# Kernel tuning notes

Measured on AMD Instinct MI355X. Metric: run time of the kernel, lower is better.

The kernel has to match this reference:

```python
import jax, jax.numpy as jnp
import numpy as np
from jax import lax

H, W = 128, 128
K_JUNC = 300
STEPS = 32
THRESH = 0.008
BIAS_SPAN = 1
SCALE = 5.0
SENTINEL = K_JUNC * K_JUNC


def decode_hafm(angs, dist, bias):
    # angs [B,3,H,W], dist [B,1,H,W], bias [B,1,H,W] -> lines [B,3,H,W,4]
    bias_range = jnp.arange(-BIAS_SPAN, BIAS_SPAN + 1, dtype=jnp.float32).reshape(1, -1, 1, 1)
    d = jnp.clip(dist + bias * bias_range, 0.0, 1.0)  # [B,3,H,W]
    angle0 = (angs[:, 0:1] - 0.5) * jnp.pi * 2
    angle1 = angs[:, 1:2] * jnp.pi / 2
    angle2 = -angs[:, 2:3] * jnp.pi / 2
    c0, s0 = jnp.cos(angle0), jnp.sin(angle0)
    t1, t2 = jnp.tan(angle1), jnp.tan(angle2)
    x1 = (c0 - s0 * t1) * d * SCALE
    y1 = (s0 + c0 * t1) * d * SCALE
    x2 = (c0 - s0 * t2) * d * SCALE
    y2 = (s0 + c0 * t2) * d * SCALE
    y0, x0 = jnp.meshgrid(jnp.arange(H, dtype=jnp.float32), jnp.arange(W, dtype=jnp.float32), indexing='ij')
    x0 = x0[None, None]
    y0 = y0[None, None]
    x1 = jnp.clip(x1 + x0, 0, W - 1)
    y1 = jnp.clip(y1 + y0, 0, H - 1)
    x2 = jnp.clip(x2 + x0, 0, W - 1)
    y2 = jnp.clip(y2 + y0, 0, H - 1)
    return jnp.stack((x1, y1, x2, y2), axis=-1)


def propose_junctions(jloc, joff):
    # jloc [H,W], joff [2,H,W]; 3x3 NMS + top-K, thresholded junctions
    pooled = lax.reduce_window(jloc, -jnp.inf, lax.max, (3, 3), (1, 1), 'SAME')
    nms = jnp.where(jloc == pooled, jloc, 0.0)
    scores, idx = lax.top_k(nms.reshape(-1), K_JUNC)
    y = (idx // W).astype(jnp.float32)
    x = (idx % W).astype(jnp.float32)
    xs = x + joff[0].reshape(-1)[idx]
    ys = y + joff[1].reshape(-1)[idx]
    coords = jnp.stack([xs, ys], axis=-1)  # [K,2]
    valid = scores > THRESH
    coords = jnp.where(valid[:, None], coords, 1e6)
    return coords, scores


def bilinear_sample(fmap, px, py):
    # fmap [C,H,W]; px,py [N,S] -> [C,N,S]
    C = fmap.shape[0]
    px = jnp.clip(px, 0.0, W - 1)
    py = jnp.clip(py, 0.0, H - 1)
    x0 = jnp.floor(px)
    y0 = jnp.floor(py)
    x0i = x0.astype(jnp.int32)
    y0i = y0.astype(jnp.int32)
    x1i = jnp.minimum(x0i + 1, W - 1)
    y1i = jnp.minimum(y0i + 1, H - 1)
    wx = px - x0
    wy = py - y0
    flat = fmap.reshape(C, H * W)

    def g(yi, xi):
        return flat[:, (yi * W + xi).reshape(-1)].reshape(C, *px.shape)

    return (g(y0i, x0i) * (1 - wx) * (1 - wy)
            + g(y0i, x1i) * wx * (1 - wy)
            + g(y1i, x0i) * (1 - wx) * wy
            + g(y1i, x1i) * wx * wy)


def setup_inputs() -> dict:
    key = jax.random.key(0)
    ks = jax.random.split(key, 10)
    return {
        'features': jax.random.normal(ks[0], (1, 256, H, W), jnp.float32),
        'heatmaps': jax.random.normal(ks[1], (1, 9, H, W), jnp.float32),
        'fc1_w': jax.random.normal(ks[2], (128, 256), jnp.float32) * 0.05,
        'fc1_b': jax.random.normal(ks[3], (128,), jnp.float32) * 0.05,
        'w1': jax.random.normal(ks[4], (1024, 1024), jnp.float32) * 0.03,
        'b1': jnp.zeros((1024,), jnp.float32),
        'w2': jax.random.normal(ks[5], (1024, 1024), jnp.float32) * 0.03,
        'b2': jnp.zeros((1024,), jnp.float32),
        'w3': jax.random.normal(ks[6], (1, 1024), jnp.float32) * 0.03,
        'b3': jnp.zeros((1,), jnp.float32),
    }


def reference(features, heatmaps, fc1_w, fc1_b, w1, b1, w2, b2, w3, b3):
    angs = jax.nn.sigmoid(heatmaps[:, 0:3])
    dist = jax.nn.sigmoid(heatmaps[:, 3:4])
    bias = jax.nn.sigmoid(heatmaps[:, 4:5])
    jloc = jax.nn.softmax(heatmaps[:, 5:7], axis=1)[0, 1]  # [H,W]
    joff = jax.nn.sigmoid(heatmaps[0, 7:9])                # [2,H,W]

    junc, _ = propose_junctions(jloc, joff)                # [K,2]
    lines = decode_hafm(angs, dist, bias).reshape(-1, 4)   # [N,4], N=3*H*W
    N = lines.shape[0]

    # junction-to-endpoint matching (cdist + argmin)
    d1 = ((junc[:, None, :] - lines[None, :, :2]) ** 2).sum(-1)  # [K,N]
    d2 = ((junc[:, None, :] - lines[None, :, 2:]) ** 2).sum(-1)
    j1 = jnp.argmin(d1, axis=0)
    j2 = jnp.argmin(d2, axis=0)
    lo = jnp.minimum(j1, j2)
    hi = jnp.maximum(j1, j2)
    ids = jnp.where(lo < hi, lo * K_JUNC + hi, SENTINEL)
    # fixed-size dedup (masked analogue of torch unique(dim=0))
    uids = jnp.unique(ids, size=N, fill_value=SENTINEL)
    valid = uids < SENTINEL
    uids_safe = jnp.where(valid, uids, 0)
    p1 = junc[uids_safe // K_JUNC]
    p2 = junc[uids_safe % K_JUNC]
    line_coords = jnp.where(valid[:, None], jnp.concatenate([p1, p2], axis=-1), 0.0)  # [N,4]

    # LOI feature sampling
    loi = jnp.einsum('oc,chw->ohw', fc1_w, features[0]) + fc1_b[:, None, None]  # [128,H,W]
    t = jnp.linspace(0.0, 1.0, STEPS)[None, :]
    px = line_coords[:, 0:1] * t + line_coords[:, 2:3] * (1 - t)  # [N,32]
    py = line_coords[:, 1:2] * t + line_coords[:, 3:4] * (1 - t)
    feats = bilinear_sample(loi, px, py)            # [128,N,32]
    feats = feats.transpose(1, 0, 2)                # [N,128,32]
    feats = feats.reshape(N, 128, STEPS // 4, 4).max(-1)  # max_pool1d k=4
    feats = feats.reshape(N, 1024)

    h = jax.nn.relu(feats @ w1.T + b1)
    h = jax.nn.relu(h @ w2.T + b2)
    logits = (h @ w3.T + b3)[:, 0]
    line_scores = jax.nn.sigmoid(logits) * valid
    return line_coords, line_scores
```

## Files before the change

kernel.cpp:

```cpp
#include <hip/hip_runtime.h>
#include <math.h>

#define HH 128
#define WW 128
#define HW 16384
#define NLINES 49152
#define KJ 300
#define SENT 90000
#define THRESHV 0.008f
#define CAND_CAP 4096
#define BITWORDS 2816

typedef __attribute__((ext_vector_type(8))) short bf16x8;
typedef __attribute__((ext_vector_type(4))) float f32x4;

__device__ __forceinline__ float sigm(float x){ return 1.0f/(1.0f+expf(-x)); }

__device__ __forceinline__ short tobf(float f){
  unsigned u = __float_as_uint(f);
  unsigned r = u + 0x7FFFu + ((u >> 16) & 1u);
  return (short)(r >> 16);
}
__device__ __forceinline__ float bflo(unsigned u){ return __uint_as_float(u << 16); }
__device__ __forceinline__ float bfhi(unsigned u){ return __uint_as_float(u & 0xFFFF0000u); }

#define GLOAD_LDS16(g, l) \
  __builtin_amdgcn_global_load_lds((const __attribute__((address_space(1))) void*)(g), \
                                   (__attribute__((address_space(3))) void*)(l), 16, 0, 0)

__device__ __forceinline__ float jloc_at(const float* hm, int idx){
  float h5 = hm[5*HW + idx], h6 = hm[6*HW + idx];
  float mx = fmaxf(h5,h6);
  float e5 = expf(h5-mx), e6 = expf(h6-mx);
  return e6/(e5+e6);
}

__global__ __launch_bounds__(256) void k_front(const float* __restrict__ hm,
    const float* __restrict__ feat, const float* __restrict__ fc1w,
    float* __restrict__ lines, unsigned long long* __restrict__ cand,
    int* __restrict__ cand_count, short* __restrict__ featT, short* __restrict__ fc1b16,
    float* __restrict__ outZero){
  __shared__ float tile[32][33];
  __shared__ float jl[4][128];
  int b = blockIdx.x, t = threadIdx.x;
  if (b < 64){
    int i = b*256 + t;
    float h0 = hm[i], h1 = hm[HW+i], h2 = hm[2*HW+i], h3 = hm[3*HW+i], h4 = hm[4*HW+i];
    float a0 = sigm(h0), a1 = sigm(h1), a2 = sigm(h2);
    float dist = sigm(h3), bias = sigm(h4);
    const float PI = 3.14159265358979323846f;
    float ang0 = (a0-0.5f)*(2.0f*PI);
    float c0 = cosf(ang0), s0 = sinf(ang0);
    float t1 = tanf(a1*(0.5f*PI));
    float t2 = tanf(-a2*(0.5f*PI));
    int y = i >> 7, x = i & 127;
    float fx = (float)x, fy = (float)y;
    #pragma unroll
    for (int c=0;c<3;c++){
      float d = fminf(fmaxf(dist + bias*(float)(c-1), 0.0f), 1.0f);
      float ds = d*5.0f;
      float x1 = fminf(fmaxf((c0 - s0*t1)*ds + fx, 0.0f), 127.0f);
      float y1 = fminf(fmaxf((s0 + c0*t1)*ds + fy, 0.0f), 127.0f);
      float x2 = fminf(fmaxf((c0 - s0*t2)*ds + fx, 0.0f), 127.0f);
      float y2 = fminf(fmaxf((s0 + c0*t2)*ds + fy, 0.0f), 127.0f);
      ((float4*)lines)[c*HW + i] = make_float4(x1,y1,x2,y2);
    }
    int y0 = 2*b;
    #pragma unroll
    for (int idx = t; idx < 512; idx += 256){
      int r = idx >> 7, xx = idx & 127;
      int yy = y0 - 1 + r;
      jl[r][xx] = (yy >= 0 && yy < HH) ? jloc_at(hm, yy*WW + xx) : -1e30f;
    }
    __syncthreads();
    int lr = 1 + (t >> 7);
    float v = jl[lr][x];
    float m = v;
    #pragma unroll
    for (int dy=-1; dy<=1; dy++){
      #pragma unroll
      for (int dx=-1; dx<=1; dx++){
        int nx = x + dx; if (nx < 0 || nx >= WW) continue;
        m = fmaxf(m, jl[lr+dy][nx]);
      }
    }
    if (v == m && v > THRESHV){
      int pos = atomicAdd(cand_count, 1);
      if (pos < CAND_CAP){
        unsigned int vb = __float_as_uint(v);
        cand[pos] = ((unsigned long long)vb << 32) | (unsigned long long)(0xFFFFFFFFu - (unsigned)i);
      }
    }
  } else if (b < 64 + 4096){
    int idx = b - 64;
    int p0 = (idx & 511) * 32, c0 = (idx >> 9) * 32;
    int c  = t >> 3;
    int p4 = (t & 7) * 4;
    float4 v = *(const float4*)&feat[(size_t)(c0 + c)*HW + p0 + p4];
    tile[c][p4+0] = v.x; tile[c][p4+1] = v.y; tile[c][p4+2] = v.z; tile[c][p4+3] = v.w;
    __syncthreads();
    int p  = t >> 3;
    int cg = (t & 7) * 4;
    ushort4 o;
    o.x = (unsigned short)tobf(tile[cg+0][p]);
    o.y = (unsigned short)tobf(tile[cg+1][p]);
    o.z = (unsigned short)tobf(tile[cg+2][p]);
    o.w = (unsigned short)tobf(tile[cg+3][p]);
    *(ushort4*)&featT[(size_t)(p0 + p)*256 + c0 + cg] = o;
  } else if (b < 4288){
    int j = (b - 4160)*256 + t;
    fc1b16[j] = tobf(fc1w[j]);
  } else {
    int j = (b - 4288)*256 + t;
    ((float4*)outZero)[j] = make_float4(0.f,0.f,0.f,0.f);
  }
}

__global__ __launch_bounds__(1024) void k_mid(
    const unsigned long long* __restrict__ cand, const int* __restrict__ cand_count,
    const float* __restrict__ hm, float* __restrict__ junc,
    const short* __restrict__ featT, const short* __restrict__ fc1b16,
    const float* __restrict__ fc1b, short* __restrict__ loi){
  __shared__ __align__(16) char smem[CAND_CAP*8];
  int b = blockIdx.x, t = threadIdx.x;
  if (b == 0){
    unsigned long long* s = (unsigned long long*)smem;
    int count = *cand_count; if (count > CAND_CAP) count = CAND_CAP;
    int n2 = 512;
    while (n2 < count) n2 <<= 1;
    for (int i=t; i<n2; i+=1024) s[i] = (i < count) ? cand[i] : 0ull;
    __syncthreads();
    for (int k=2; k<=n2; k<<=1){
      for (int j=k>>1; j>0; j>>=1){
        for (int i=t; i<n2; i+=1024){
          int ixj = i ^ j;
          if (ixj > i){
            unsigned long long a = s[i], bb = s[ixj];
            bool desc = ((i & k) == 0);
            if (desc ? (a < bb) : (a > bb)){ s[i] = bb; s[ixj] = a; }
          }
        }
        __syncthreads();
      }
    }
    if (t < KJ){
      float jx = 1e6f, jy = 1e6f;
      if (t < count){
        unsigned idx = 0xFFFFFFFFu - (unsigned)(s[t] & 0xFFFFFFFFull);
        int yy = (int)(idx >> 7), xx = (int)(idx & 127u);
        jx = (float)xx + sigm(hm[7*HW + idx]);
        jy = (float)yy + sigm(hm[8*HW + idx]);
      }
      junc[2*t] = jx; junc[2*t+1] = jy;
    }
  } else {
    if (t >= 256) return;
    short* As = (short*)smem;
    short* Bs = (short*)(smem + 8192);
    int rb = (b - 1) * 64;
    int lane = t & 63, wave = t >> 6;
    int l16 = lane & 15, quad = lane >> 4;
    int srow = lane >> 3, schunk = (lane & 7) ^ srow;
    f32x4 acc[8];
    #pragma unroll
    for (int g=0; g<8; g++) acc[g] = (f32x4){0,0,0,0};
    for (int k0=0; k0<256; k0+=64){
      #pragma unroll
      for (int i=0; i<2; i++){
        int r0 = wave*16 + i*8;
        GLOAD_LDS16(featT + (size_t)(rb + r0 + srow)*256 + k0 + schunk*8, &As[r0*64]);
      }
      #pragma unroll
      for (int i=0; i<4; i++){
        int r0 = wave*32 + i*8;
        GLOAD_LDS16(fc1b16 + (size_t)(r0 + srow)*256 + k0 + schunk*8, &Bs[r0*64]);
      }
      __syncthreads();
      #pragma unroll
      for (int s2=0; s2<2; s2++){
        int slot = (s2*4 + quad) ^ (l16 & 7);
        bf16x8 a = *(const bf16x8*)&As[(wave*16 + l16)*64 + slot*8];
        #pragma unroll
        for (int g=0; g<8; g++){
          bf16x8 bv = *(const bf16x8*)&Bs[(g*16 + l16)*64 + slot*8];
          acc[g] = __builtin_amdgcn_mfma_f32_16x16x32_bf16(a, bv, acc[g], 0, 0, 0);
        }
      }
      __syncthreads();
    }
    int rowbase = rb + wave*16 + quad*4;
    #pragma unroll
    for (int g=0; g<8; g++){
      int col = g*16 + l16;
      float bs = fc1b[col];
      #pragma unroll
      for (int r=0; r<4; r++)
        loi[(size_t)(rowbase + r)*128 + col] = tobf(acc[g][r] + bs);
    }
  }
}

__global__ __launch_bounds__(256) void k_match(const float* __restrict__ lines,
    const float* __restrict__ junc, unsigned* __restrict__ bm,
    const float* __restrict__ w1, const float* __restrict__ w2,
    short* __restrict__ w1b, short* __restrict__ w2b){
  __shared__ float jx[KJ], jy[KJ];
  int b = blockIdx.x, t = threadIdx.x;
  if (b < 192){
    for (int k=t; k<KJ; k+=256){ jx[k] = junc[2*k]; jy[k] = junc[2*k+1]; }
    __syncthreads();
    int n = b*256 + t;
    float4 L = ((const float4*)lines)[n];
    float b1 = 1e30f, b2 = 1e30f; int j1 = 0, j2 = 0;
    #pragma unroll 4
    for (int k=0; k<KJ; k++){
      float dx1 = jx[k]-L.x, dy1 = jy[k]-L.y;
      float d1 = dx1*dx1 + dy1*dy1;
      float dx2 = jx[k]-L.z, dy2 = jy[k]-L.w;
      float d2 = dx2*dx2 + dy2*dy2;
      if (d1 < b1){ b1 = d1; j1 = k; }
      if (d2 < b2){ b2 = d2; j2 = k; }
    }
    int lo = min(j1,j2), hi = max(j1,j2);
    if (lo < hi){
      int id = lo*KJ + hi;
      atomicOr(&bm[id >> 5], 1u << (id & 31));
    }
  } else {
    int j = (b - 192)*256 + t;
    w1b[j] = tobf(w1[j]);
    w2b[j] = tobf(w2[j]);
  }
}

__global__ __launch_bounds__(1024) void k_unique(const unsigned* __restrict__ bm,
    int* __restrict__ uid_list, int* __restrict__ mcount){
  __shared__ int wsum[16];
  int t = threadIdx.x;
  int w0 = t*3;
  unsigned wv[3];
  int local = 0;
  #pragma unroll
  for (int i=0; i<3; i++){
    int w = w0 + i;
    wv[i] = (w < BITWORDS) ? bm[w] : 0u;
    local += __popc(wv[i]);
  }
  int v = local;
  #pragma unroll
  for (int d=1; d<64; d<<=1){
    int nv = __shfl_up(v, d, 64);
    if ((t & 63) >= d) v += nv;
  }
  if ((t & 63) == 63) wsum[t >> 6] = v;
  __syncthreads();
  if (t < 16){
    int x = wsum[t];
    #pragma unroll
    for (int d=1; d<16; d<<=1){
      int nv = __shfl_up(x, d, 16);
      if (t >= d) x += nv;
    }
    wsum[t] = x;
  }
  __syncthreads();
  int base = v - local + ((t >> 6) ? wsum[(t >> 6) - 1] : 0);
  #pragma unroll
  for (int i=0; i<3; i++){
    unsigned bits = wv[i];
    while (bits){
      int bb = __ffs(bits) - 1;
      uid_list[base++] = (w0 + i)*32 + bb;
      bits &= bits - 1;
    }
  }
  if (t == 1023) *mcount = wsum[15];
}

__global__ __launch_bounds__(256) void k_sample(float* __restrict__ out,
    const int* __restrict__ uid_list, const float* __restrict__ junc,
    const short* __restrict__ loi, const int* __restrict__ mcount,
    short* __restrict__ fbuf, float* __restrict__ logit, int chunk0, int chunk){
  __shared__ int4   sOffs[2][32];
  __shared__ float4 sWts[2][32];
  int M = *mcount;
  int t = threadIdx.x;
  int q  = t >> 6;
  int c2 = (t & 63) << 1;
  int lim = M - chunk0; if (lim > chunk) lim = chunk;
  for (int l0 = blockIdx.x*2; l0 < lim; l0 += gridDim.x*2){
    __syncthreads();
    if (t < 64){
      int pair = t >> 5, s = t & 31;
      int l = l0 + pair;
      if (l < lim){
        int r = chunk0 + l;
        int id = uid_list[r];
        int lo = id / KJ, hi = id % KJ;
        float2 P1 = ((const float2*)junc)[lo];
        float2 P2 = ((const float2*)junc)[hi];
        if (s == 0){
          ((float4*)out)[r] = make_float4(P1.x, P1.y, P2.x, P2.y);
          logit[l] = 0.0f;
        }
        float tt = (float)s * (1.0f/31.0f);
        float px = P1.x*tt + P2.x*(1.0f-tt);
        float py = P1.y*tt + P2.y*(1.0f-tt);
        px = fminf(fmaxf(px, 0.0f), 127.0f);
        py = fminf(fmaxf(py, 0.0f), 127.0f);
        float x0 = floorf(px), y0 = floorf(py);
        int x0i = (int)x0, y0i = (int)y0;
        int x1i = min(x0i+1, 127), y1i = min(y0i+1, 127);
        float wx = px - x0, wy = py - y0;
        sOffs[pair][s] = make_int4((y0i*WW + x0i)*128, (y0i*WW + x1i)*128,
                                   (y1i*WW + x0i)*128, (y1i*WW + x1i)*128);
        sWts[pair][s]  = make_float4((1.0f-wx)*(1.0f-wy), wx*(1.0f-wy),
                                     (1.0f-wx)*wy,        wx*wy);
      }
    }
    __syncthreads();
    #pragma unroll
    for (int pair=0; pair<2; pair++){
      int l = l0 + pair;
      if (l >= lim) break;
      float gl0=-1e30f, gl1=-1e30f, gh0=-1e30f, gh1=-1e30f;
      #pragma unroll
      for (int j=0; j<8; j++){
        int s = q*8 + j;
        int4 o   = sOffs[pair][s];
        float4 w = sWts[pair][s];
        unsigned u00 = *(const unsigned*)&loi[o.x + c2];
        unsigned u01 = *(const unsigned*)&loi[o.y + c2];
        unsigned u10 = *(const unsigned*)&loi[o.z + c2];
        unsigned u11 = *(const unsigned*)&loi[o.w + c2];
        float vlo = w.x*bflo(u00) + w.y*bflo(u01) + w.z*bflo(u10) + w.w*bflo(u11);
        float vhi = w.x*bfhi(u00) + w.y*bfhi(u01) + w.z*bfhi(u10) + w.w*bfhi(u11);
        if (j < 4){ gl0 = fmaxf(gl0, vlo); gh0 = fmaxf(gh0, vhi); }
        else      { gl1 = fmaxf(gl1, vlo); gh1 = fmaxf(gh1, vhi); }
      }
      unsigned plo = ((unsigned)(unsigned short)tobf(gl0)) | (((unsigned)(unsigned short)tobf(gl1)) << 16);
      unsigned phi = ((unsigned)(unsigned short)tobf(gh0)) | (((unsigned)(unsigned short)tobf(gh1)) << 16);
      *(unsigned*)&fbuf[(size_t)l*1024 + c2*8 + q*2]     = plo;
      *(unsigned*)&fbuf[(size_t)l*1024 + (c2+1)*8 + q*2] = phi;
    }
  }
}

template<int MODE>
__global__ __launch_bounds__(256) void k_mlp(const short* __restrict__ A,
    const short* __restrict__ B, const float* __restrict__ bias,
    short* __restrict__ Hout, const float* __restrict__ w3,
    float* __restrict__ logit, const int* __restrict__ mcount, int chunk0){
  int M = *mcount;
  int rb = blockIdx.x * 64;
  if (chunk0 + rb >= M) return;
  int cb = blockIdx.y * 128;
  __shared__ short As[64*64];
  __shared__ short Bs[128*64];
  int lane = threadIdx.x & 63, wave = threadIdx.x >> 6;
  int l16 = lane & 15, quad = lane >> 4;
  int srow = lane >> 3, schunk = (lane & 7) ^ srow;
  f32x4 acc[8];
  #pragma unroll
  for (int g=0; g<8; g++) acc[g] = (f32x4){0,0,0,0};
  for (int k0=0; k0<1024; k0+=64){
    #pragma unroll
    for (int i=0; i<2; i++){
      int r0 = wave*16 + i*8;
      GLOAD_LDS16(A + (size_t)(rb + r0 + srow)*1024 + k0 + schunk*8, &As[r0*64]);
    }
    #pragma unroll
    for (int i=0; i<4; i++){
      int r0 = wave*32 + i*8;
      GLOAD_LDS16(B + (size_t)(cb + r0 + srow)*1024 + k0 + schunk*8, &Bs[r0*64]);
    }
    __syncthreads();
    #pragma unroll
    for (int s=0; s<2; s++){
      int slot = (s*4 + quad) ^ (l16 & 7);
      bf16x8 a = *(const bf16x8*)&As[(wave*16 + l16)*64 + slot*8];
      #pragma unroll
      for (int g=0; g<8; g++){
        bf16x8 bv = *(const bf16x8*)&Bs[(g*16 + l16)*64 + slot*8];
        acc[g] = __builtin_amdgcn_mfma_f32_16x16x32_bf16(a, bv, acc[g], 0, 0, 0);
      }
    }
    __syncthreads();
  }
  int rowbase = rb + wave*16 + quad*4;
  if (MODE == 0){
    #pragma unroll
    for (int g=0; g<8; g++){
      int col = cb + g*16 + l16;
      float bs = bias[col];
      #pragma unroll
      for (int r=0; r<4; r++)
        Hout[(size_t)(rowbase + r)*1024 + col] = tobf(fmaxf(acc[g][r] + bs, 0.0f));
    }
  } else {
    float p0[4] = {0,0,0,0};
    #pragma unroll
    for (int g=0; g<8; g++){
      int col = cb + g*16 + l16;
      float bs = bias[col], wv = w3[col];
      #pragma unroll
      for (int r=0; r<4; r++)
        p0[r] += fmaxf(acc[g][r] + bs, 0.0f) * wv;
    }
    #pragma unroll
    for (int r=0; r<4; r++){
      #pragma unroll
      for (int m=1; m<16; m<<=1)
        p0[r] += __shfl_xor(p0[r], m, 16);
    }
    if (l16 == 0){
      #pragma unroll
      for (int r=0; r<4; r++)
        atomicAdd(&logit[rowbase + r], p0[r]);
    }
  }
}

__global__ void k_score(const float* __restrict__ logit, const float* __restrict__ b3,
                        const int* __restrict__ mcount, float* __restrict__ out, int chunk0){
  int i = blockIdx.x*blockDim.x + threadIdx.x;
  int r = chunk0 + i;
  int M = *mcount;
  if (r >= M) return;
  float lg = logit[i] + b3[0];
  out[4*NLINES + r] = 1.0f/(1.0f + expf(-lg));
}

extern "C" void kernel_launch(void* const* d_in, const int* in_sizes, int n_in,
                              void* d_out, int out_size, void* d_ws, size_t ws_size,
                              hipStream_t stream){
  const float* features = (const float*)d_in[0];
  const float* heatmaps = (const float*)d_in[1];
  const float* fc1_w    = (const float*)d_in[2];
  const float* fc1_b    = (const float*)d_in[3];
  const float* w1       = (const float*)d_in[4];
  const float* b1       = (const float*)d_in[5];
  const float* w2       = (const float*)d_in[6];
  const float* b2       = (const float*)d_in[7];
  const float* w3       = (const float*)d_in[8];
  const float* b3       = (const float*)d_in[9];
  float* out = (float*)d_out;

  char* ws = (char*)d_ws;
  size_t off = 0;
  auto alloc = [&](size_t bytes) -> void* {
    void* p = ws + off;
    off = (off + bytes + 255) & ~(size_t)255;
    return p;
  };
  float* lines     = (float*)alloc((size_t)NLINES*16);
  unsigned long long* cand = (unsigned long long*)alloc(CAND_CAP*8);
  int*      cand_count = (int*)alloc(4);
  unsigned* bitmap     = (unsigned*)alloc(BITWORDS*4);
  size_t zlen = (size_t)((char*)(bitmap + BITWORDS) - (char*)cand_count);
  float* junc      = (float*)alloc(KJ*2*4);
  int*   uid_list  = (int*)alloc((size_t)45056*4);
  int*   mcount    = (int*)alloc(4);
  short* loi       = (short*)alloc((size_t)HW*128*2);
  short* featT     = (short*)alloc((size_t)HW*256*2);
  short* fc1b16    = (short*)alloc((size_t)128*256*2);
  short* w1b       = (short*)alloc((size_t)1024*1024*2);
  short* w2b       = (short*)alloc((size_t)1024*1024*2);
  size_t fixed = off;

  const int chunk_opts[4] = {45056, 22528, 11264, 5632};
  int CHUNK = 5632;
  for (int ci=0; ci<4; ci++){
    size_t need = fixed + (size_t)chunk_opts[ci]*1024*2*2 + (size_t)chunk_opts[ci]*4 + 1024;
    if (need <= ws_size){ CHUNK = chunk_opts[ci]; break; }
  }
  short* fbuf  = (short*)alloc((size_t)CHUNK*1024*2);
  short* h1buf = (short*)alloc((size_t)CHUNK*1024*2);
  float* logit = (float*)alloc((size_t)CHUNK*4);

  hipMemsetAsync(cand_count, 0, zlen, stream);
  k_front<<<4528, 256, 0, stream>>>(heatmaps, features, fc1_w, lines, cand,
                                    cand_count, featT, fc1b16, out);
  k_mid  <<<257, 1024, 0, stream>>>(cand, cand_count, heatmaps, junc, featT,
                                    fc1b16, fc1_b, loi);
  k_match<<<4288, 256, 0, stream>>>(lines, junc, bitmap, w1, w2, w1b, w2b);
  k_unique<<<1, 1024, 0, stream>>>(bitmap, uid_list, mcount);

  int nchunk = (45056 + CHUNK - 1) / CHUNK;
  for (int ci=0; ci<nchunk; ci++){
    int chunk0 = ci * CHUNK;
    k_sample<<<1024, 256, 0, stream>>>(out, uid_list, junc, loi, mcount, fbuf,
                                       logit, chunk0, CHUNK);
    dim3 g1(CHUNK/64, 8);
    k_mlp<0><<<g1, 256, 0, stream>>>(fbuf, w1b, b1, h1buf, nullptr,
                                     nullptr, mcount, chunk0);
    k_mlp<2><<<g1, 256, 0, stream>>>(h1buf, w2b, b2, nullptr, w3,
                                     logit, mcount, chunk0);
    k_score<<<(CHUNK+255)/256, 256, 0, stream>>>(logit, b3, mcount, out, chunk0);
  }
}
```

Baseline: 199.6 us.

## Replace full bitonic sort of junction candidates with histogram radix-select prefilter

Block 0 of k_mid used to bitonic-sort every junction candidate (up to 4096) to find the top 300. It now builds an 11-bit histogram of the key's top bits, finds the boundary bin with a suffix scan, and compacts only the candidates at or above that bin into a small buffer. Only that subset is sorted, with the old full sort kept as a fallback when more than 2048 survive. The aim is to shorten the serial top-K critical path on one block, at the cost of extra atomics, scans and more code.

```diff
diff --git a/kernel.cpp b/kernel.cpp
--- a/kernel.cpp
+++ b/kernel.cpp
@@ -122,36 +122,113 @@
     const short* __restrict__ featT, const short* __restrict__ fc1b16,
     const float* __restrict__ fc1b, short* __restrict__ loi){
   __shared__ __align__(16) char smem[CAND_CAP*8];
+  __shared__ int wsum16[16];
+  __shared__ int sBbin, sScnt;
   int b = blockIdx.x, t = threadIdx.x;
   if (b == 0){
-    unsigned long long* s = (unsigned long long*)smem;
+    int* hist = (int*)smem;
+    unsigned long long* sel = (unsigned long long*)(smem + 8192);
+    unsigned long long* sfull = (unsigned long long*)smem;
     int count = *cand_count; if (count > CAND_CAP) count = CAND_CAP;
-    int n2 = 512;
-    while (n2 < count) n2 <<= 1;
-    for (int i=t; i<n2; i+=1024) s[i] = (i < count) ? cand[i] : 0ull;
-    __syncthreads();
-    for (int k=2; k<=n2; k<<=1){
-      for (int j=k>>1; j>0; j>>=1){
-        for (int i=t; i<n2; i+=1024){
-          int ixj = i ^ j;
-          if (ixj > i){
-            unsigned long long a = s[i], bb = s[ixj];
-            bool desc = ((i & k) == 0);
-            if (desc ? (a < bb) : (a > bb)){ s[i] = bb; s[ixj] = a; }
+    int need = count < KJ ? count : KJ;
+    hist[t] = 0; hist[t + 1024] = 0;
+    if (t == 0){ sScnt = 0; sBbin = -1; }
+    __syncthreads();
+    for (int i=t; i<count; i+=1024){
+      int bin = (int)(cand[i] >> 52) & 0x7FF;
+      atomicAdd(&hist[bin], 1);
+    }
+    __syncthreads();
+    int c0 = hist[2*t], c1 = hist[2*t+1];
+    int pairv = c0 + c1;
+    int v = pairv;
+    #pragma unroll
+    for (int d=1; d<64; d<<=1){
+      int nv = __shfl_down(v, d, 64);
+      if ((t & 63) + d < 64) v += nv;
+    }
+    if ((t & 63) == 0) wsum16[t >> 6] = v;
+    __syncthreads();
+    if (t < 16){
+      int x = wsum16[t];
+      #pragma unroll
+      for (int d=1; d<16; d<<=1){
+        int nv = __shfl_down(x, d, 16);
+        if (t + d < 16) x += nv;
+      }
+      wsum16[t] = x;
+    }
+    __syncthreads();
+    int w = t >> 6;
+    int after = (w < 15) ? wsum16[w+1] : 0;
+    int suf = v + after;
+    int A_hi = suf - pairv;
+    int A_lo = A_hi + c1;
+    if (need > 0){
+      if (A_hi < need && need <= A_hi + c1)      sBbin = 2*t+1;
+      else if (A_lo < need && need <= A_lo + c0) sBbin = 2*t;
+    }
+    __syncthreads();
+    int Bbin = sBbin;
+    if (Bbin >= 0){
+      for (int i=t; i<count; i+=1024){
+        unsigned long long k = cand[i];
+        int bin = (int)(k >> 52) & 0x7FF;
+        if (bin >= Bbin){
+          int p = atomicAdd(&sScnt, 1);
+          if (p < 2048) sel[p] = k;
+        }
+      }
+    }
+    __syncthreads();
+    int S = sScnt;
+    bool fb = (S > 2048);
+    if (!fb){
+      int n2 = 512; while (n2 < S) n2 <<= 1;
+      for (int i=t; i<n2; i+=1024) if (i >= S) sel[i] = 0ull;
+      __syncthreads();
+      for (int k=2; k<=n2; k<<=1){
+        for (int j=k>>1; j>0; j>>=1){
+          for (int i=t; i<n2; i+=1024){
+            int ixj = i ^ j;
+            if (ixj > i){
+              unsigned long long a = sel[i], bb = sel[ixj];
+              bool desc = ((i & k) == 0);
+              if (desc ? (a < bb) : (a > bb)){ sel[i] = bb; sel[ixj] = a; }
+            }
           }
+          __syncthreads();
         }
-        __syncthreads();
+      }
+    } else {
+      int n2 = 512; while (n2 < count) n2 <<= 1;
+      __syncthreads();
+      for (int i=t; i<n2; i+=1024) sfull[i] = (i < count) ? cand[i] : 0ull;
+      __syncthreads();
+      for (int k=2; k<=n2; k<<=1){
+        for (int j=k>>1; j>0; j>>=1){
+          for (int i=t; i<n2; i+=1024){
+            int ixj = i ^ j;
+            if (ixj > i){
+              unsigned long long a = sfull[i], bb = sfull[ixj];
+              bool desc = ((i & k) == 0);
+              if (desc ? (a < bb) : (a > bb)){ sfull[i] = bb; sfull[ixj] = a; }
+            }
+          }
+          __syncthreads();
+        }
       }
     }
     if (t < KJ){
-      float jx = 1e6f, jy = 1e6f;
+      float jxv = 1e6f, jyv = 1e6f;
       if (t < count){
-        unsigned idx = 0xFFFFFFFFu - (unsigned)(s[t] & 0xFFFFFFFFull);
+        unsigned long long kk = fb ? sfull[t] : sel[t];
+        unsigned idx = 0xFFFFFFFFu - (unsigned)(kk & 0xFFFFFFFFull);
         int yy = (int)(idx >> 7), xx = (int)(idx & 127u);
-        jx = (float)xx + sigm(hm[7*HW + idx]);
-        jy = (float)yy + sigm(hm[8*HW + idx]);
-      }
-      junc[2*t] = jx; junc[2*t+1] = jy;
+        jxv = (float)xx + sigm(hm[7*HW + idx]);
+        jyv = (float)yy + sigm(hm[8*HW + idx]);
+      }
+      junc[2*t] = jxv; junc[2*t+1] = jyv;
     }
   } else {
     if (t >= 256) return;
```

Measured after the change: 180.9 us, median of 2. -9.3%, faster.
